# Kernel optimization log

Measured on AMD Instinct MI355X. Metric: run time of the kernel, lower is better.

The kernel has to match this reference:

```python
import jax, jax.numpy as jnp
import numpy as np
from jax.scipy.linalg import expm

DIM = 128      # state matrix size
DEPTH = 16     # max path length for positions < 2**16
N = 8192       # number of unique positions
MAXPOS = 65536


def setup_inputs() -> dict:
    key = jax.random.key(0)
    k1, k2 = jax.random.split(key)
    unique = jax.random.randint(k1, (N,), 1, MAXPOS, dtype=jnp.int32)
    # matches torch init: rand -> softmax(-1) -> cumsum(-1)
    primitives_raw = jnp.cumsum(
        jax.nn.softmax(jax.random.uniform(k2, (2, DIM, DIM), dtype=jnp.float32), axis=-1),
        axis=-1)
    identity = jnp.eye(DIM, dtype=jnp.float32)[None]  # [1, dim, dim]
    return {"unique": unique, "primitives_raw": primitives_raw, "identity": identity}


def _path_bits(pos, depth):
    # pos_to_path(idx): bits idx%2, (idx//2)%2, ... up to (but excluding) the leading 1.
    # bit k is valid iff (pos >> k) > 1; invalid slots get padding value 2 (-> identity map).
    k = jnp.arange(depth, dtype=pos.dtype)
    v = pos[:, None] >> k[None, :]                 # [N, depth]
    return jnp.where(v > 1, v & 1, 2).astype(jnp.int32)


def reference(unique, primitives_raw, identity):
    # primitives = matrix_exp(P - P^H)  (real params -> plain transpose)
    herm = primitives_raw - jnp.swapaxes(primitives_raw, -1, -2)
    prim = jax.vmap(expm)(herm)                                        # [2, dim, dim]
    eye = jnp.eye(DIM, dtype=prim.dtype)[None]
    pstack = jnp.concatenate([prim, eye], axis=0)                      # [3, dim, dim]; index 2 = padding/no-op
    bits = _path_bits(unique, DEPTH)                                   # [N, DEPTH]
    n = unique.shape[0]
    maps0 = jnp.broadcast_to(identity.astype(prim.dtype), (n, DIM, DIM))

    def step(maps, b):
        # linear(maps, W) == maps @ W.T, with per-position W selected by the path bit
        w = pstack[b]                                                  # [N, dim, dim]
        return jnp.einsum('naj,nij->nai', maps, w), None

    maps, _ = jax.lax.scan(step, maps0, bits.T)                        # scan over depth
    return maps
```

## Files before the change

kernel.cpp:

```cpp
#include <hip/hip_runtime.h>

#define DIM   128
#define MSZ   (DIM*DIM)


__global__ __launch_bounds__(256) void k_herm(const float* __restrict__ P,
                                              double* __restrict__ dbuf) {
  const int b = blockIdx.y;
  const float* Pb = P + b * MSZ;
  double* H = dbuf + (size_t)(0*2 + b) * MSZ;
  for (int idx = blockIdx.x*256 + threadIdx.x; idx < MSZ; idx += 32*256) {
    const int x = idx >> 7, y = idx & 127;
    H[idx] = ((double)Pb[y*DIM + x] - (double)Pb[x*DIM + y]) * (1.0/256.0);
  }
}

__global__ __launch_bounds__(256) void k_mm64(double* __restrict__ dbuf,
                                              int ds, int as, int bs, int adds) {
  const int b = blockIdx.y;
  const double* A = dbuf + (size_t)(as*2 + b) * MSZ;
  const double* B = dbuf + (size_t)(bs*2 + b) * MSZ;
  double*       C = dbuf + (size_t)(ds*2 + b) * MSZ;
  const int idx = blockIdx.x*256 + threadIdx.x;
  const int i = idx >> 7, j = idx & 127;
  const double* Ar = A + i*DIM;
  double a0 = 0.0, a1 = 0.0, a2 = 0.0, a3 = 0.0;
  #pragma unroll 4
  for (int k = 0; k < DIM; k += 4) {
    a0 = fma(Ar[k+0], B[(k+0)*DIM + j], a0);
    a1 = fma(Ar[k+1], B[(k+1)*DIM + j], a1);
    a2 = fma(Ar[k+2], B[(k+2)*DIM + j], a2);
    a3 = fma(Ar[k+3], B[(k+3)*DIM + j], a3);
  }
  double acc = (a0 + a1) + (a2 + a3);
  if (adds >= 0) acc += (dbuf + (size_t)(adds*2 + b)*MSZ)[idx];
  C[idx] = acc;
}

__global__ __launch_bounds__(256) void k_qelem(double* __restrict__ dbuf) {
  const int b = blockIdx.y;
  const double *H  = dbuf + (size_t)(0*2+b)*MSZ, *H2 = dbuf + (size_t)(1*2+b)*MSZ,
               *H3 = dbuf + (size_t)(2*2+b)*MSZ, *H4 = dbuf + (size_t)(3*2+b)*MSZ,
               *H5 = dbuf + (size_t)(4*2+b)*MSZ;
  double *Q0 = dbuf + (size_t)(5*2+b)*MSZ, *R = dbuf + (size_t)(6*2+b)*MSZ;
  for (int idx = blockIdx.x*256 + threadIdx.x; idx < MSZ; idx += 32*256) {
    const double di = ((idx >> 7) == (idx & 127)) ? 1.0 : 0.0;
    const double h = H[idx], h2 = H2[idx], h3 = H3[idx], h4 = H4[idx], h5 = H5[idx];
    Q0[idx] = di + h + h2*(1.0/2.0) + h3*(1.0/6.0) + h4*(1.0/24.0);
    R[idx]  = di*(1.0/120.0) + h*(1.0/720.0) + h2*(1.0/5040.0)
            + h3*(1.0/40320.0) + h4*(1.0/362880.0) + h5*(1.0/3628800.0);
  }
}

__global__ __launch_bounds__(256) void k_finalize(const double* __restrict__ dbuf,
                                                  float* __restrict__ T) {
  const int role = blockIdx.y;
  if (role == 2) {
    for (int idx = blockIdx.x*256 + threadIdx.x; idx < MSZ; idx += 32*256)
      T[(size_t)1*MSZ + idx] = ((idx >> 7) == (idx & 127)) ? 1.0f : 0.0f;
  } else {
    const double* E = dbuf + (size_t)(7*2 + role)*MSZ;
    float* dst = T + (size_t)(2 + role)*MSZ;
    for (int idx = blockIdx.x*256 + threadIdx.x; idx < MSZ; idx += 32*256)
      dst[idx] = (float)E[idx];
  }
}

__device__ __forceinline__ void mm128f(const float* __restrict__ A,
                                       const float* __restrict__ Bg,
                                       float* __restrict__ C) {
  __shared__ float Bs[MSZ];
  for (int idx = threadIdx.x*4; idx < MSZ; idx += 256*4)
    *(float4*)&Bs[idx] = *(const float4*)&Bg[idx];
  __syncthreads();

  const int t  = threadIdx.x;
  const int i0 = (t >> 4) << 3;
  const int j0 = (t & 15) << 3;

  float acc[8][8];
  #pragma unroll
  for (int r = 0; r < 8; ++r)
    #pragma unroll
    for (int c = 0; c < 8; ++c) acc[r][c] = 0.0f;

  for (int k = 0; k < DIM; k += 4) {
    alignas(16) float aa[8][4];
    #pragma unroll
    for (int r = 0; r < 8; ++r)
      *(float4*)&aa[r][0] = *(const float4*)&A[(i0 + r)*DIM + k];
    #pragma unroll
    for (int kk = 0; kk < 4; ++kk) {
      alignas(16) float bb[8];
      *(float4*)&bb[0] = *(const float4*)&Bs[(k + kk)*DIM + j0];
      *(float4*)&bb[4] = *(const float4*)&Bs[(k + kk)*DIM + j0 + 4];
      #pragma unroll
      for (int r = 0; r < 8; ++r) {
        const float ar = aa[r][kk];
        #pragma unroll
        for (int c = 0; c < 8; ++c) acc[r][c] = fmaf(ar, bb[c], acc[r][c]);
      }
    }
  }

  #pragma unroll
  for (int r = 0; r < 8; ++r) {
    *(float4*)&C[(i0 + r)*DIM + j0]
        = make_float4(acc[r][0], acc[r][1], acc[r][2], acc[r][3]);
    *(float4*)&C[(i0 + r)*DIM + j0 + 4]
        = make_float4(acc[r][4], acc[r][5], acc[r][6], acc[r][7]);
  }
}

__global__ __launch_bounds__(256) void k_jobs(float* __restrict__ T, int wave) {
  const int j = blockIdx.x;
  int dst, a, b;
  if (wave == 0)      { dst = 4 + j;   a = 2 + (j & 1);  b = 2 + (j >> 1); }
  else if (wave == 1) {
    if (j < 8)        { dst = 8 + j;   a = 2 + (j & 1);  b = 4 + (j >> 1); }
    else { const int m = j - 8;   dst = 16 + m;  a = 4 + (m & 3);  b = 4 + (m >> 2); }
  } else {
    if (j < 32)       { const int m = j;       dst = 32 + m;  a = 2 + (m & 1);  b = 16 + (m >> 1); }
    else if (j < 96)  { const int m = j - 32;  dst = 64 + m;  a = 4 + (m & 3);  b = 16 + (m >> 2); }
    else if (j < 224) { const int m = j - 96;  dst = 128 + m; a = 8 + (m & 7);  b = 16 + (m >> 3); }
    else              { const int m = j - 224; dst = 256 + m; a = 16 + (m & 15); b = 16 + (m >> 4); }
  }
  mm128f(T + (size_t)a*MSZ, T + (size_t)b*MSZ, T + (size_t)dst*MSZ);
}

__global__ __launch_bounds__(256) void k_final(const float* __restrict__ T,
                                               const int* __restrict__ unique,
                                               float* __restrict__ out) {
  const int n   = blockIdx.x;
  int pos = unique[n];
  pos = (pos < 1) ? 1 : (pos & 0xFFFF);
  const int hi  = pos >> 8;
  const int ai  = (hi == 0) ? pos : (256 | (pos & 255));
  const int bi  = (hi == 0) ? 1 : hi;
  mm128f(T + (size_t)ai*MSZ, T + (size_t)bi*MSZ, out + (size_t)n*MSZ);
}

extern "C" void kernel_launch(void* const* d_in, const int* in_sizes, int n_in,
                              void* d_out, int out_size, void* d_ws, size_t ws_size,
                              hipStream_t stream) {
  const int*   unique = (const int*)d_in[0];
  const float* praw   = (const float*)d_in[1];
  const int n = in_sizes[0];
  double* dbuf = (double*)d_ws;
  float*  T    = (float*)((char*)d_ws + (4u << 20));
  float*  out  = (float*)d_out;

  k_herm <<<dim3(32,2),256,0,stream>>>(praw, dbuf);
  k_mm64 <<<dim3(64,2),256,0,stream>>>(dbuf, 1,0,0, -1);
  k_mm64 <<<dim3(64,2),256,0,stream>>>(dbuf, 2,1,0, -1);
  k_mm64 <<<dim3(64,2),256,0,stream>>>(dbuf, 3,1,1, -1);
  k_mm64 <<<dim3(64,2),256,0,stream>>>(dbuf, 4,1,2, -1);
  k_qelem<<<dim3(32,2),256,0,stream>>>(dbuf);
  k_mm64 <<<dim3(64,2),256,0,stream>>>(dbuf, 7,6,4, 5);
  int cur = 7;
  for (int s = 0; s < 8; ++s) {
    const int nxt = cur ^ 1;
    k_mm64<<<dim3(64,2),256,0,stream>>>(dbuf, nxt, cur, cur, -1);
    cur = nxt;
  }
  k_finalize<<<dim3(32,3),256,0,stream>>>(dbuf, T);

  k_jobs<<<dim3(4),  256,0,stream>>>(T, 0);
  k_jobs<<<dim3(24), 256,0,stream>>>(T, 1);
  k_jobs<<<dim3(480),256,0,stream>>>(T, 2);

  k_final<<<dim3(n),256,0,stream>>>(T, unique, out);
}
```

Before: 1.076 ms.

## Use bf16x3 split MFMA matmuls for product table and final outputs

```diff
diff --git a/kernel.cpp b/kernel.cpp
--- a/kernel.cpp
+++ b/kernel.cpp
@@ -1,7 +1,12 @@
 #include <hip/hip_runtime.h>
+#include <hip/hip_bf16.h>
 
 #define DIM   128
 #define MSZ   (DIM*DIM)
+
+typedef __attribute__((ext_vector_type(8))) short          v8s;
+typedef __attribute__((ext_vector_type(4))) float          f32x4;
+typedef __attribute__((ext_vector_type(8))) unsigned short u16x8;
 
 
 __global__ __launch_bounds__(256) void k_herm(const float* __restrict__ P,
@@ -52,6 +57,182 @@
   }
 }
 
+__device__ __forceinline__ unsigned short bf16_bits(float f) {
+  union { __hip_bfloat16 b; unsigned short u; } cv;
+  cv.b = __float2bfloat16(f);
+  return cv.u;
+}
+__device__ __forceinline__ float bf16_back(unsigned short u) {
+  union { __hip_bfloat16 b; unsigned short u; } cv;
+  cv.u = u;
+  return __bfloat162float(cv.b);
+}
+__device__ __forceinline__ void split3(float x, unsigned short& u0,
+                                       unsigned short& u1, unsigned short& u2) {
+  u0 = bf16_bits(x);              float f0 = bf16_back(u0);
+  u1 = bf16_bits(x - f0);         float f1 = bf16_back(u1);
+  u2 = bf16_bits(x - f0 - f1);
+}
+
+#define T3_ENT  512
+#define T3T_ENT 256
+
+__global__ __launch_bounds__(256) void k_finalize_splits(const double* __restrict__ dbuf,
+                                                         unsigned short* __restrict__ T3,
+                                                         unsigned short* __restrict__ T3T) {
+  const int role = blockIdx.y;
+  const int ent  = (role == 2) ? 1 : (2 + role);
+  const double* E = dbuf + (size_t)(7*2 + (role & 1)) * MSZ;
+  for (int idx = blockIdx.x*256 + threadIdx.x; idx < MSZ; idx += 32*256) {
+    const int row = idx >> 7, col = idx & 127;
+    const float x = (role == 2) ? ((row == col) ? 1.0f : 0.0f) : (float)E[idx];
+    unsigned short u0, u1, u2;
+    split3(x, u0, u1, u2);
+    const size_t e3  = (size_t)ent * MSZ + idx;
+    const size_t e3t = (size_t)ent * MSZ + col*DIM + row;
+    T3 [(size_t)0*T3_ENT*MSZ  + e3 ] = u0;
+    T3 [(size_t)1*T3_ENT*MSZ  + e3 ] = u1;
+    T3 [(size_t)2*T3_ENT*MSZ  + e3 ] = u2;
+    T3T[(size_t)0*T3T_ENT*MSZ + e3t] = u0;
+    T3T[(size_t)1*T3T_ENT*MSZ + e3t] = u1;
+    T3T[(size_t)2*T3T_ENT*MSZ + e3t] = u2;
+  }
+}
+
+__device__ __forceinline__ void mm_mfma_core(const unsigned short* __restrict__ T3,
+                                             const unsigned short* __restrict__ T3T,
+                                             int ea, int eb,
+                                             unsigned short* __restrict__ smem,
+                                             f32x4 (&acc)[2][8]) {
+  const int t   = threadIdx.x;
+  const int w   = t >> 6;
+  const int l   = t & 63;
+  const int l15 = l & 15;
+  const int g   = l >> 4;
+
+  #pragma unroll
+  for (int tr = 0; tr < 2; ++tr)
+    #pragma unroll
+    for (int tc = 0; tc < 8; ++tc) acc[tr][tc] = (f32x4)(0.0f);
+
+  #pragma unroll
+  for (int q = 0; q < 3; ++q) {
+    const unsigned short* src = T3T + ((size_t)q * T3T_ENT + eb) * MSZ;
+    #pragma unroll
+    for (int it = 0; it < 8; ++it) {
+      const int e   = (it*256 + t) * 8;
+      const int col = e >> 7;
+      int off = col*256 + (e & 127)*2;
+      off ^= (col & 15) << 4;
+      *(u16x8*)((char*)smem + off) = *(const u16x8*)(src + e);
+    }
+    __syncthreads();
+
+    #pragma unroll
+    for (int ks = 0; ks < 4; ++ks) {
+      v8s bf[8];
+      #pragma unroll
+      for (int tc = 0; tc < 8; ++tc) {
+        const int col = tc*16 + l15;
+        int off = col*256 + ks*64 + g*16;
+        off ^= (col & 15) << 4;
+        bf[tc] = *(const v8s*)((const char*)smem + off);
+      }
+      v8s af[3][2];
+      #pragma unroll
+      for (int p = 0; p < 3 - q; ++p) {
+        const unsigned short* ap = T3 + ((size_t)p * T3_ENT + ea) * MSZ;
+        #pragma unroll
+        for (int tr = 0; tr < 2; ++tr) {
+          const int row = w*32 + tr*16 + l15;
+          af[p][tr] = *(const v8s*)(ap + row*DIM + ks*32 + g*8);
+        }
+      }
+      #pragma unroll
+      for (int p = 0; p < 3 - q; ++p)
+        #pragma unroll
+        for (int tr = 0; tr < 2; ++tr)
+          #pragma unroll
+          for (int tc = 0; tc < 8; ++tc)
+            acc[tr][tc] = __builtin_amdgcn_mfma_f32_16x16x32_bf16(
+                              af[p][tr], bf[tc], acc[tr][tc], 0, 0, 0);
+    }
+    __syncthreads();
+  }
+}
+
+__global__ __launch_bounds__(256, 2) void k_jobs_mfma(unsigned short* __restrict__ T3,
+                                                      unsigned short* __restrict__ T3T,
+                                                      int wave) {
+  const int j = blockIdx.x;
+  int dst, a, b;
+  if (wave == 0)      { dst = 4 + j;   a = 2 + (j & 1);  b = 2 + (j >> 1); }
+  else if (wave == 1) {
+    if (j < 8)        { dst = 8 + j;   a = 2 + (j & 1);  b = 4 + (j >> 1); }
+    else { const int m = j - 8;   dst = 16 + m;  a = 4 + (m & 3);  b = 4 + (m >> 2); }
+  } else {
+    if (j < 32)       { const int m = j;       dst = 32 + m;  a = 2 + (m & 1);  b = 16 + (m >> 1); }
+    else if (j < 96)  { const int m = j - 32;  dst = 64 + m;  a = 4 + (m & 3);  b = 16 + (m >> 2); }
+    else if (j < 224) { const int m = j - 96;  dst = 128 + m; a = 8 + (m & 7);  b = 16 + (m >> 3); }
+    else              { const int m = j - 224; dst = 256 + m; a = 16 + (m & 15); b = 16 + (m >> 4); }
+  }
+  __shared__ unsigned short smem[MSZ];
+  f32x4 acc[2][8];
+  mm_mfma_core(T3, T3T, a, b, smem, acc);
+
+  const int t = threadIdx.x, w = t >> 6, l = t & 63, l15 = l & 15, g = l >> 4;
+  #pragma unroll
+  for (int tr = 0; tr < 2; ++tr)
+    #pragma unroll
+    for (int tc = 0; tc < 8; ++tc)
+      #pragma unroll
+      for (int r = 0; r < 4; ++r) {
+        const int row = w*32 + tr*16 + g*4 + r;
+        const int col = tc*16 + l15;
+        unsigned short u0, u1, u2;
+        split3(acc[tr][tc][r], u0, u1, u2);
+        const size_t e3 = (size_t)dst * MSZ + row*DIM + col;
+        T3[(size_t)0*T3_ENT*MSZ + e3] = u0;
+        T3[(size_t)1*T3_ENT*MSZ + e3] = u1;
+        T3[(size_t)2*T3_ENT*MSZ + e3] = u2;
+        if (dst < T3T_ENT) {
+          const size_t e3t = (size_t)dst * MSZ + col*DIM + row;
+          T3T[(size_t)0*T3T_ENT*MSZ + e3t] = u0;
+          T3T[(size_t)1*T3T_ENT*MSZ + e3t] = u1;
+          T3T[(size_t)2*T3T_ENT*MSZ + e3t] = u2;
+        }
+      }
+}
+
+__global__ __launch_bounds__(256, 2) void k_final_mfma(const unsigned short* __restrict__ T3,
+                                                       const unsigned short* __restrict__ T3T,
+                                                       const int* __restrict__ unique,
+                                                       float* __restrict__ out) {
+  const int n = blockIdx.x;
+  int pos = unique[n];
+  pos = (pos < 1) ? 1 : (pos & 0xFFFF);
+  const int hi = pos >> 8;
+  const int ea = hi ? (256 | (pos & 255)) : pos;
+  const int eb = hi ? hi : 1;
+
+  __shared__ unsigned short smem[MSZ];
+  f32x4 acc[2][8];
+  mm_mfma_core(T3, T3T, ea, eb, smem, acc);
+
+  const int t = threadIdx.x, w = t >> 6, l = t & 63, l15 = l & 15, g = l >> 4;
+  float* o = out + (size_t)n * MSZ;
+  #pragma unroll
+  for (int tr = 0; tr < 2; ++tr)
+    #pragma unroll
+    for (int tc = 0; tc < 8; ++tc)
+      #pragma unroll
+      for (int r = 0; r < 4; ++r) {
+        const int row = w*32 + tr*16 + g*4 + r;
+        const int col = tc*16 + l15;
+        o[row*DIM + col] = acc[tr][tc][r];
+      }
+}
+
 __global__ __launch_bounds__(256) void k_finalize(const double* __restrict__ dbuf,
                                                   float* __restrict__ T) {
   const int role = blockIdx.y;
@@ -73,17 +254,14 @@
   for (int idx = threadIdx.x*4; idx < MSZ; idx += 256*4)
     *(float4*)&Bs[idx] = *(const float4*)&Bg[idx];
   __syncthreads();
-
   const int t  = threadIdx.x;
   const int i0 = (t >> 4) << 3;
   const int j0 = (t & 15) << 3;
-
   float acc[8][8];
   #pragma unroll
   for (int r = 0; r < 8; ++r)
     #pragma unroll
     for (int c = 0; c < 8; ++c) acc[r][c] = 0.0f;
-
   for (int k = 0; k < DIM; k += 4) {
     alignas(16) float aa[8][4];
     #pragma unroll
@@ -102,7 +280,6 @@
       }
     }
   }
-
   #pragma unroll
   for (int r = 0; r < 8; ++r) {
     *(float4*)&C[(i0 + r)*DIM + j0]
@@ -147,7 +324,6 @@
   const float* praw   = (const float*)d_in[1];
   const int n = in_sizes[0];
   double* dbuf = (double*)d_ws;
-  float*  T    = (float*)((char*)d_ws + (4u << 20));
   float*  out  = (float*)d_out;
 
   k_herm <<<dim3(32,2),256,0,stream>>>(praw, dbuf);
@@ -163,11 +339,23 @@
     k_mm64<<<dim3(64,2),256,0,stream>>>(dbuf, nxt, cur, cur, -1);
     cur = nxt;
   }
-  k_finalize<<<dim3(32,3),256,0,stream>>>(dbuf, T);
-
-  k_jobs<<<dim3(4),  256,0,stream>>>(T, 0);
-  k_jobs<<<dim3(24), 256,0,stream>>>(T, 1);
-  k_jobs<<<dim3(480),256,0,stream>>>(T, 2);
-
-  k_final<<<dim3(n),256,0,stream>>>(T, unique, out);
-}
+
+  const size_t NEED = (size_t)76 << 20;
+  if (ws_size >= NEED) {
+    unsigned short* T3  = (unsigned short*)((char*)d_ws + ((size_t)4 << 20));
+    unsigned short* T3T = T3 + (size_t)3 * T3_ENT * MSZ;
+
+    k_finalize_splits<<<dim3(32,3),256,0,stream>>>(dbuf, T3, T3T);
+    k_jobs_mfma<<<dim3(4),  256,0,stream>>>(T3, T3T, 0);
+    k_jobs_mfma<<<dim3(24), 256,0,stream>>>(T3, T3T, 1);
+    k_jobs_mfma<<<dim3(480),256,0,stream>>>(T3, T3T, 2);
+    k_final_mfma<<<dim3(n),256,0,stream>>>(T3, T3T, unique, out);
+  } else {
+    float* T = (float*)((char*)d_ws + ((size_t)4 << 20));
+    k_finalize<<<dim3(32,3),256,0,stream>>>(dbuf, T);
+    k_jobs<<<dim3(4),  256,0,stream>>>(T, 0);
+    k_jobs<<<dim3(24), 256,0,stream>>>(T, 1);
+    k_jobs<<<dim3(480),256,0,stream>>>(T, 2);
+    k_final<<<dim3(n),256,0,stream>>>(T, unique, out);
+  }
+}
```

Result: faster. 1.001 ms (-7.0%).
